# Performance work log

Measured on AMD Instinct MI355X. Metric: run time of the kernel, lower is better.

Reference implementation:

```python
import jax, jax.numpy as jnp
import numpy as np

IMAGE_SIZE = 256
NEAR = 0.1
FAR = 100.0
EPS = 1e-3
BACKGROUND = (0.0, 0.0, 0.0)
CHUNK = 64   # faces per scan step (bounds peak memory of the z-buffer pass)
TINY = 1e-12


def _bary(vx, vy, vz, xp, yp):
    """Barycentric weights / perspective-correct depth at pixel centers.
    vx, vy, vz: 3-tuples of vertex coords, broadcastable with xp/yp.
    Mirrors the CUDA kernel: unnormalized cross-product weights, normalize,
    clamp to [0,1], renormalize, zp = 1 / sum(w_k / z_k), near/far clip."""
    x0, x1, x2 = vx; y0, y1, y2 = vy; z0, z1, z2 = vz
    w0 = yp * (x2 - x1) + xp * (y1 - y2) + (x1 * y2 - x2 * y1)
    w1 = yp * (x0 - x2) + xp * (y2 - y0) + (x2 * y0 - x0 * y2)
    w2 = yp * (x1 - x0) + xp * (y0 - y1) + (x0 * y1 - x1 * y0)
    det = w0 + w1 + w2
    safe_det = jnp.where(jnp.abs(det) > TINY, det, 1.0)
    n0, n1, n2 = w0 / safe_det, w1 / safe_det, w2 / safe_det
    inside = (n0 > 0) & (n1 > 0) & (n2 > 0) & (jnp.abs(det) > TINY)
    n0 = jnp.clip(n0, 0.0, 1.0); n1 = jnp.clip(n1, 0.0, 1.0); n2 = jnp.clip(n2, 0.0, 1.0)
    s = n0 + n1 + n2
    s = jnp.where(s > TINY, s, 1.0)
    n0, n1, n2 = n0 / s, n1 / s, n2 / s
    inv_zp = n0 / z0 + n1 / z1 + n2 / z2
    inv_zp = jnp.where(jnp.abs(inv_zp) > TINY, inv_zp, 1.0)
    zp = 1.0 / inv_zp
    valid = inside & (zp > NEAR) & (zp < FAR)
    return (n0, n1, n2), zp, valid


def _pixel_coords():
    IS = IMAGE_SIZE
    return (2.0 * jnp.arange(IS, dtype=jnp.float32) + 1.0 - IS) / IS


def _forward(faces, textures):
    B, F = faces.shape[:2]
    IS = IMAGE_SIZE
    ii = _pixel_coords()

    # ---- pass 1: z-buffer (face-index argmin), chunked scan over faces ----
    # index selection is non-differentiable -> stop_gradient keeps vjp cheap
    fsg = jax.lax.stop_gradient(faces)
    n_chunks = F // CHUNK
    fchunks = jnp.transpose(fsg.reshape(B, n_chunks, CHUNK, 3, 3), (1, 0, 2, 3, 4))
    bases = jnp.arange(n_chunks, dtype=jnp.int32) * CHUNK
    xp4 = ii[None, None, None, :]
    yp4 = ii[None, None, :, None]

    def step(carry, inp):
        depth, fidx = carry
        fc, base = inp                               # fc: [B, CHUNK, 3, 3]
        vx = tuple(fc[:, :, k, 0][:, :, None, None] for k in range(3))
        vy = tuple(fc[:, :, k, 1][:, :, None, None] for k in range(3))
        vz = tuple(fc[:, :, k, 2][:, :, None, None] for k in range(3))
        _, zp, valid = _bary(vx, vy, vz, xp4, yp4)   # [B, CHUNK, IS, IS]
        zp = jnp.where(valid, zp, jnp.inf)
        local = jnp.argmin(zp, axis=1).astype(jnp.int32)
        zbest = jnp.min(zp, axis=1)
        better = zbest < depth
        depth = jnp.where(better, zbest, depth)
        fidx = jnp.where(better, base + local, fidx)
        return (depth, fidx), None

    init = (jnp.full((B, IS, IS), FAR, jnp.float32),
            jnp.full((B, IS, IS), -1, jnp.int32))
    (_, fidx), _ = jax.lax.scan(step, init, (fchunks, bases))

    # ---- pass 2: differentiable recompute for winning faces ----
    mask = fidx >= 0
    safe_idx = jnp.maximum(fidx, 0)
    fsel = jnp.take_along_axis(
        faces.reshape(B, F, 9), safe_idx.reshape(B, -1, 1), axis=1
    ).reshape(B, IS, IS, 3, 3)
    vx = tuple(fsel[..., k, 0] for k in range(3))
    vy = tuple(fsel[..., k, 1] for k in range(3))
    vz = tuple(fsel[..., k, 2] for k in range(3))
    w, zp, _ = _bary(vx, vy, vz, ii[None, None, :], ii[None, :, None])
    depth_map = jnp.where(mask, zp, FAR)

    # ---- texture sampling: 8-corner trilinear in the T^3 face texel cube ----
    T = textures.shape[2]
    tif = [jnp.clip(w[k] * (T - 1) * zp / vz[k], 0.0, T - 1 - EPS) for k in range(3)]
    lo = [jnp.floor(t) for t in tif]
    fr = [t - l for t, l in zip(tif, lo)]
    lo = [l.astype(jnp.int32) for l in lo]

    tex_flat = textures.reshape(B, F * T * T * T, 3)
    base_idx = safe_idx * (T * T * T)
    rgb = jnp.zeros((B, IS, IS, 3), faces.dtype)
    for d0 in (0, 1):
        for d1 in (0, 1):
            for d2 in (0, 1):
                wgt = ((fr[0] if d0 else 1.0 - fr[0]) *
                       (fr[1] if d1 else 1.0 - fr[1]) *
                       (fr[2] if d2 else 1.0 - fr[2]))
                idx = base_idx + (lo[0] + d0) * T * T + (lo[1] + d1) * T + (lo[2] + d2)
                smp = jnp.take_along_axis(tex_flat, idx.reshape(B, -1, 1), axis=1)
                rgb = rgb + wgt[..., None] * smp.reshape(B, IS, IS, 3)

    bg = jnp.asarray(BACKGROUND, faces.dtype)
    mf = mask.astype(faces.dtype)[..., None]
    rgb_map = rgb * mf + (1.0 - mf) * bg
    alpha_map = mask.astype(faces.dtype)
    # pack (rgb, alpha, depth) into a single [B, IS, IS, 5] tensor
    return jnp.concatenate([rgb_map, alpha_map[..., None], depth_map[..., None]], axis=-1)


def setup_inputs() -> dict:
    key = jax.random.key(0)
    B, F, T = 4, 4096, 4
    k1, k2, k3, k4, k5 = jax.random.split(key, 5)
    # small triangles scattered over the screen with depths in (near, far)
    ctr = jax.random.uniform(k1, (B, F, 1, 2), minval=-0.95, maxval=0.95)
    off = jax.random.uniform(k2, (B, F, 3, 2), minval=-0.08, maxval=0.08)
    xy = ctr + off
    zc = jax.random.uniform(k3, (B, F, 1, 1), minval=1.0, maxval=50.0)
    zo = jax.random.uniform(k4, (B, F, 3, 1), minval=-0.2, maxval=0.2)
    faces = jnp.concatenate([xy, zc + zo], axis=-1).astype(jnp.float32)
    textures = jax.random.uniform(k5, (B, F, T, T, T, 3), dtype=jnp.float32)
    return {"faces": faces, "textures": textures}


def reference(faces, textures):
    return _forward(faces, textures)
```

## Files before the change

### kernel.cpp

```cpp
#include <hip/hip_runtime.h>

#define IS 256
#define FCOUNT 4096
#define NEARP 0.1f
#define FARP 100.0f
#define TINYF 1e-12f
#define CAP 192
#define GCAP 128
#define DET_GLOBAL 1e-5f
#define ZEPS 2e-4f

__device__ __forceinline__ float frn(float r) { asm("" : "+v"(r)); return r; }
__device__ __forceinline__ float mulrn(float a, float b) { return frn(a * b); }
__device__ __forceinline__ float addrn(float a, float b) { return frn(a + b); }
__device__ __forceinline__ float subrn(float a, float b) { return frn(a - b); }
__device__ __forceinline__ float divrn(float a, float b) { return frn(a / b); }
__device__ __forceinline__ float fmarn(float a, float b, float c) {
    return frn(__builtin_fmaf(a, b, c));
}


__global__ __launch_bounds__(64) void bin_kernel(
    const float* __restrict__ faces,
    float4* __restrict__ cA, float4* __restrict__ cB, float4* __restrict__ cC,
    int* __restrict__ counts, int* __restrict__ lists,
    int* __restrict__ gcount, int* __restrict__ glist, int B, int F)
{
    const int lane = threadIdx.x;
    const int base = blockIdx.x * 64;
    const int gid  = base + lane;
    if (gid >= B * F) return;
    const int b = gid >> 12, f = gid & (FCOUNT - 1);

    __shared__ float4 stage4[144];
    float* stage = (float*)stage4;
    const float* src = faces + (size_t)base * 9;
    const float4* s4 = (const float4*)src;
    stage4[lane]      = s4[lane];
    stage4[64 + lane] = s4[64 + lane];
    stage[512 + lane] = src[512 + lane];
    __builtin_amdgcn_wave_barrier();

    const float* fp = stage + lane * 9;
    const float x0 = fp[0], y0 = fp[1], z0 = fp[2];
    const float x1 = fp[3], y1 = fp[4], z1 = fp[5];
    const float x2 = fp[6], y2 = fp[7], z2 = fp[8];

    const float A0 = subrn(x2, x1), B0 = subrn(y1, y2);
    const float C0 = fmarn(x1, y2, -mulrn(x2, y1));
    const float A1 = subrn(x0, x2), B1 = subrn(y2, y0);
    const float C1 = fmarn(x2, y0, -mulrn(x0, y2));
    const float A2 = subrn(x1, x0), B2 = subrn(y0, y1);
    const float C2 = fmarn(x0, y1, -mulrn(x1, y0));
    cA[gid] = make_float4(A0, B0, C0, A1);
    cB[gid] = make_float4(B1, C1, A2, B2);
    cC[gid] = make_float4(C2, z0, z1, z2);

    const float det = (x1 - x0) * (y2 - y0) - (x2 - x0) * (y1 - y0);
    const float ad = fabsf(det);
    if (ad < DET_GLOBAL) {
        const int pos = atomicAdd(&gcount[b], 1);
        if (pos < GCAP) glist[b * GCAP + pos] = f;
        return;
    }
    const float d = 2e-3f + 3e-7f / ad;
    const float lox = fminf(x0, fminf(x1, x2)) - d;
    const float hix = fmaxf(x0, fmaxf(x1, x2)) + d;
    const float loy = fminf(y0, fminf(y1, y2)) - d;
    const float hiy = fmaxf(y0, fmaxf(y1, y2)) + d;
    int tx0 = (int)ceilf ((256.f * lox + 241.f) * (1.f / 16.f));
    int tx1 = (int)floorf((256.f * hix + 255.f) * (1.f / 16.f));
    int ty0 = (int)ceilf ((256.f * loy + 241.f) * (1.f / 16.f));
    int ty1 = (int)floorf((256.f * hiy + 255.f) * (1.f / 16.f));
    tx0 = max(tx0, 0); tx1 = min(tx1, 31);
    ty0 = max(ty0, 0); ty1 = min(ty1, 31);
    for (int ty = ty0; ty <= ty1; ++ty)
        for (int tx = tx0; tx <= tx1; ++tx) {
            const int t = (b * 32 + ty) * 32 + tx;
            const int pos = atomicAdd(&counts[t], 1);
            if (pos < CAP) lists[(size_t)t * CAP + pos] = f;
        }
}

__global__ __launch_bounds__(64) void raster_kernel(
    const float* __restrict__ textures,
    const float4* __restrict__ cA, const float4* __restrict__ cB,
    const float4* __restrict__ cC,
    const int* __restrict__ counts, const int* __restrict__ lists,
    const int* __restrict__ gcount, const int* __restrict__ glist,
    float* __restrict__ out, int B, int F)
{
    const int lane = threadIdx.x;
    const int blk  = blockIdx.x;
    const int b    = blk >> 10;
    const int tx   = blk & 31;
    const int ty   = (blk >> 5) & 31;
    const int bin  = (b * 32 + ty) * 32 + tx;
    const int px   = tx * 8 + (lane & 7);
    const int py   = ty * 8 + (lane >> 3);
    const float xp = (float)(2 * px + 1 - IS) * (1.0f / IS);
    const float yp = (float)(2 * py + 1 - IS) * (1.0f / IS);

    const int cnt   = min(counts[bin], CAP);
    const int gcnt  = min(gcount[b], GCAP);
    const int total = cnt + gcnt;
    const int* mylist = lists + (size_t)bin * CAP;
    const int* gl     = glist + b * GCAP;
    const int fb = b * F;

    float bestz = FARP;
    int   besti = -1;
    float bn0 = 0.f, bn1 = 0.f, bn2 = 0.f;
    float bz0 = 1.f, bz1 = 1.f, bz2 = 1.f;

    int    pf = 0;
    float4 pa, pb, pc;
    if (total > 0) {
        pf = (0 < cnt) ? mylist[0] : gl[0];
        pa = cA[fb + pf]; pb = cB[fb + pf]; pc = cC[fb + pf];
    }
    for (int j = 0; j < total; ++j) {
        const float4 fa  = pa;
        const float4 fb4 = pb;
        const float4 fc  = pc;
        const int    fi  = pf;
        const int jn = j + 1;
        if (jn < total) {
            pf = (jn < cnt) ? mylist[jn] : gl[jn - cnt];
            pa = cA[fb + pf]; pb = cB[fb + pf]; pc = cC[fb + pf];
        }
        const float w0 = addrn(fmarn(yp, fa.x, mulrn(xp, fa.y)), fa.z);
        const float w1 = addrn(fmarn(yp, fa.w, mulrn(xp, fb4.x)), fb4.y);
        const float w2 = addrn(fmarn(yp, fb4.z, mulrn(xp, fb4.w)), fc.x);
        const float det = addrn(addrn(w0, w1), w2);
        bool ins;
        if (det > TINYF)       ins = (w0 > 0.f) && (w1 > 0.f) && (w2 > 0.f);
        else if (det < -TINYF) ins = (w0 < 0.f) && (w1 < 0.f) && (w2 < 0.f);
        else                   ins = false;
        const float minz = fminf(fminf(fc.y, fc.z), fc.w);
        if (ins && minz <= bestz + ZEPS) {
            float n0 = divrn(w0, det), n1 = divrn(w1, det), n2 = divrn(w2, det);
            n0 = frn(fminf(fmaxf(n0, 0.f), 1.f));
            n1 = frn(fminf(fmaxf(n1, 0.f), 1.f));
            n2 = frn(fminf(fmaxf(n2, 0.f), 1.f));
            float s = addrn(addrn(n0, n1), n2);
            s = (s > TINYF) ? s : 1.0f;
            n0 = divrn(n0, s); n1 = divrn(n1, s); n2 = divrn(n2, s);
            float iz = addrn(addrn(divrn(n0, fc.y), divrn(n1, fc.z)),
                             divrn(n2, fc.w));
            iz = (fabsf(iz) > TINYF) ? iz : 1.0f;
            const float zp = divrn(1.0f, iz);
            if (zp > NEARP && zp < FARP) {
                if (zp < bestz || (zp == bestz && fi < besti)) {
                    bestz = zp;
                    besti = fi;
                    bn0 = n0; bn1 = n1; bn2 = n2;
                    bz0 = fc.y; bz1 = fc.z; bz2 = fc.w;
                }
            }
        }
    }

    float r = 0.f, g = 0.f, bch = 0.f, alpha = 0.f, depth = FARP;
    if (besti >= 0) {
        const float zp = bestz;
        depth = zp;
        const float t0 = fminf(fmaxf(divrn(mulrn(mulrn(bn0, 3.0f), zp), bz0), 0.f), 2.999f);
        const float t1 = fminf(fmaxf(divrn(mulrn(mulrn(bn1, 3.0f), zp), bz1), 0.f), 2.999f);
        const float t2 = fminf(fmaxf(divrn(mulrn(mulrn(bn2, 3.0f), zp), bz2), 0.f), 2.999f);
        const float l0 = floorf(t0), l1 = floorf(t1), l2 = floorf(t2);
        const float fr0 = subrn(t0, l0), fr1 = subrn(t1, l1), fr2 = subrn(t2, l2);
        const int i0 = (int)l0, i1 = (int)l1, i2 = (int)l2;

        const float* txp = textures + (size_t)(b * F + besti) * 64 * 3;
        for (int d0 = 0; d0 < 2; ++d0)
            for (int d1 = 0; d1 < 2; ++d1)
                for (int d2 = 0; d2 < 2; ++d2) {
                    const float wg = mulrn(mulrn(d0 ? fr0 : subrn(1.0f, fr0),
                                                 d1 ? fr1 : subrn(1.0f, fr1)),
                                           d2 ? fr2 : subrn(1.0f, fr2));
                    const float* tp = txp + ((i0 + d0) * 16 + (i1 + d1) * 4 + (i2 + d2)) * 3;
                    r   = addrn(r,   mulrn(wg, tp[0]));
                    g   = addrn(g,   mulrn(wg, tp[1]));
                    bch = addrn(bch, mulrn(wg, tp[2]));
                }
        alpha = 1.0f;
    }

    float* op = out + (((size_t)b * IS + py) * IS + px) * 5;
    op[0] = r;
    op[1] = g;
    op[2] = bch;
    op[3] = alpha;
    op[4] = depth;
}

extern "C" void kernel_launch(void* const* d_in, const int* in_sizes, int n_in,
                              void* d_out, int out_size, void* d_ws, size_t ws_size,
                              hipStream_t stream) {
    const float* faces    = (const float*)d_in[0];
    const float* textures = (const float*)d_in[1];
    float* out = (float*)d_out;
    const int F = FCOUNT;
    const int B = in_sizes[0] / (F * 9);
    const int nbins = B * 1024;

    int* counts = (int*)d_ws;
    int* gcount = counts + nbins;
    int* glist  = gcount + B;
    int* lists  = glist + B * GCAP;
    float4* cA  = (float4*)(lists + (size_t)nbins * CAP);
    float4* cB  = cA + (size_t)B * F;
    float4* cC  = cB + (size_t)B * F;

    hipMemsetAsync(counts, 0, (size_t)(nbins + B) * sizeof(int), stream);
    bin_kernel<<<dim3((B * F + 63) / 64), dim3(64), 0, stream>>>(
        faces, cA, cB, cC, counts, lists, gcount, glist, B, F);
    raster_kernel<<<dim3(B * 1024), dim3(64), 0, stream>>>(
        textures, cA, cB, cC, counts, lists, gcount, glist, out, B, F);
}
```

Before: 103.7 us.

## Split per-tile face list across four waves and merge depth winners in shared memory

The raster kernel now runs four wavefronts per 8x8 tile. Each wave scans every fourth face in the bin list and keeps its own best depth. The per-wave winners go to LDS, and wave 0 reduces them with the same tie-break on lower face index, then does texture sampling and output. This shortens the serial per-pixel loop over candidate faces. The cost is a block barrier, LDS traffic, and idle waves during shading. The early-out on bestz is also weaker, since each wave only sees its own subset of faces.

```diff
diff --git a/kernel.cpp b/kernel.cpp
--- a/kernel.cpp
+++ b/kernel.cpp
@@ -82,7 +82,7 @@
         }
 }
 
-__global__ __launch_bounds__(64) void raster_kernel(
+__global__ __launch_bounds__(256, 8) void raster_kernel(
     const float* __restrict__ textures,
     const float4* __restrict__ cA, const float4* __restrict__ cB,
     const float4* __restrict__ cC,
@@ -90,7 +90,9 @@
     const int* __restrict__ gcount, const int* __restrict__ glist,
     float* __restrict__ out, int B, int F)
 {
-    const int lane = threadIdx.x;
+    const int tid  = threadIdx.x;
+    const int lane = tid & 63;
+    const int w    = tid >> 6;
     const int blk  = blockIdx.x;
     const int b    = blk >> 10;
     const int tx   = blk & 31;
@@ -101,6 +103,11 @@
     const float xp = (float)(2 * px + 1 - IS) * (1.0f / IS);
     const float yp = (float)(2 * py + 1 - IS) * (1.0f / IS);
 
+    __shared__ float s_pz[4][64];
+    __shared__ int   s_pi[4][64];
+    __shared__ float s_pn[4][64][3];
+    __shared__ float s_pvz[4][64][3];
+
     const int cnt   = min(counts[bin], CAP);
     const int gcnt  = min(gcount[b], GCAP);
     const int total = cnt + gcnt;
@@ -115,16 +122,16 @@
 
     int    pf = 0;
     float4 pa, pb, pc;
-    if (total > 0) {
-        pf = (0 < cnt) ? mylist[0] : gl[0];
+    if (w < total) {
+        pf = (w < cnt) ? mylist[w] : gl[w - cnt];
         pa = cA[fb + pf]; pb = cB[fb + pf]; pc = cC[fb + pf];
     }
-    for (int j = 0; j < total; ++j) {
+    for (int j = w; j < total; j += 4) {
         const float4 fa  = pa;
         const float4 fb4 = pb;
         const float4 fc  = pc;
         const int    fi  = pf;
-        const int jn = j + 1;
+        const int jn = j + 4;
         if (jn < total) {
             pf = (jn < cnt) ? mylist[jn] : gl[jn - cnt];
             pa = cA[fb + pf]; pb = cB[fb + pf]; pc = cC[fb + pf];
@@ -161,38 +168,62 @@
         }
     }
 
-    float r = 0.f, g = 0.f, bch = 0.f, alpha = 0.f, depth = FARP;
-    if (besti >= 0) {
-        const float zp = bestz;
-        depth = zp;
-        const float t0 = fminf(fmaxf(divrn(mulrn(mulrn(bn0, 3.0f), zp), bz0), 0.f), 2.999f);
-        const float t1 = fminf(fmaxf(divrn(mulrn(mulrn(bn1, 3.0f), zp), bz1), 0.f), 2.999f);
-        const float t2 = fminf(fmaxf(divrn(mulrn(mulrn(bn2, 3.0f), zp), bz2), 0.f), 2.999f);
-        const float l0 = floorf(t0), l1 = floorf(t1), l2 = floorf(t2);
-        const float fr0 = subrn(t0, l0), fr1 = subrn(t1, l1), fr2 = subrn(t2, l2);
-        const int i0 = (int)l0, i1 = (int)l1, i2 = (int)l2;
-
-        const float* txp = textures + (size_t)(b * F + besti) * 64 * 3;
-        for (int d0 = 0; d0 < 2; ++d0)
-            for (int d1 = 0; d1 < 2; ++d1)
-                for (int d2 = 0; d2 < 2; ++d2) {
-                    const float wg = mulrn(mulrn(d0 ? fr0 : subrn(1.0f, fr0),
-                                                 d1 ? fr1 : subrn(1.0f, fr1)),
-                                           d2 ? fr2 : subrn(1.0f, fr2));
-                    const float* tp = txp + ((i0 + d0) * 16 + (i1 + d1) * 4 + (i2 + d2)) * 3;
-                    r   = addrn(r,   mulrn(wg, tp[0]));
-                    g   = addrn(g,   mulrn(wg, tp[1]));
-                    bch = addrn(bch, mulrn(wg, tp[2]));
-                }
-        alpha = 1.0f;
-    }
-
-    float* op = out + (((size_t)b * IS + py) * IS + px) * 5;
-    op[0] = r;
-    op[1] = g;
-    op[2] = bch;
-    op[3] = alpha;
-    op[4] = depth;
+    s_pz[w][lane] = bestz;
+    s_pi[w][lane] = besti;
+    s_pn[w][lane][0]  = bn0; s_pn[w][lane][1]  = bn1; s_pn[w][lane][2]  = bn2;
+    s_pvz[w][lane][0] = bz0; s_pvz[w][lane][1] = bz1; s_pvz[w][lane][2] = bz2;
+    __syncthreads();
+
+    if (w == 0) {
+        float z = s_pz[0][lane];
+        int   i = s_pi[0][lane];
+        int  ws = 0;
+        #pragma unroll
+        for (int s = 1; s < 4; ++s) {
+            const float zs = s_pz[s][lane];
+            const int   is = s_pi[s][lane];
+            if (zs < z || (zs == z && is < i)) { z = zs; i = is; ws = s; }
+        }
+
+        float r = 0.f, g = 0.f, bch = 0.f, alpha = 0.f, depth = FARP;
+        if (i >= 0) {
+            const float n0 = s_pn[ws][lane][0];
+            const float n1 = s_pn[ws][lane][1];
+            const float n2 = s_pn[ws][lane][2];
+            const float z0 = s_pvz[ws][lane][0];
+            const float z1 = s_pvz[ws][lane][1];
+            const float z2 = s_pvz[ws][lane][2];
+            const float zp = z;
+            depth = zp;
+            const float t0 = fminf(fmaxf(divrn(mulrn(mulrn(n0, 3.0f), zp), z0), 0.f), 2.999f);
+            const float t1 = fminf(fmaxf(divrn(mulrn(mulrn(n1, 3.0f), zp), z1), 0.f), 2.999f);
+            const float t2 = fminf(fmaxf(divrn(mulrn(mulrn(n2, 3.0f), zp), z2), 0.f), 2.999f);
+            const float l0 = floorf(t0), l1 = floorf(t1), l2 = floorf(t2);
+            const float fr0 = subrn(t0, l0), fr1 = subrn(t1, l1), fr2 = subrn(t2, l2);
+            const int i0 = (int)l0, i1 = (int)l1, i2 = (int)l2;
+
+            const float* txp = textures + (size_t)(b * F + i) * 64 * 3;
+            for (int d0 = 0; d0 < 2; ++d0)
+                for (int d1 = 0; d1 < 2; ++d1)
+                    for (int d2 = 0; d2 < 2; ++d2) {
+                        const float wg = mulrn(mulrn(d0 ? fr0 : subrn(1.0f, fr0),
+                                                     d1 ? fr1 : subrn(1.0f, fr1)),
+                                               d2 ? fr2 : subrn(1.0f, fr2));
+                        const float* tp = txp + ((i0 + d0) * 16 + (i1 + d1) * 4 + (i2 + d2)) * 3;
+                        r   = addrn(r,   mulrn(wg, tp[0]));
+                        g   = addrn(g,   mulrn(wg, tp[1]));
+                        bch = addrn(bch, mulrn(wg, tp[2]));
+                    }
+            alpha = 1.0f;
+        }
+
+        float* op = out + (((size_t)b * IS + py) * IS + px) * 5;
+        op[0] = r;
+        op[1] = g;
+        op[2] = bch;
+        op[3] = alpha;
+        op[4] = depth;
+    }
 }
 
 extern "C" void kernel_launch(void* const* d_in, const int* in_sizes, int n_in,
@@ -216,6 +247,6 @@
     hipMemsetAsync(counts, 0, (size_t)(nbins + B) * sizeof(int), stream);
     bin_kernel<<<dim3((B * F + 63) / 64), dim3(64), 0, stream>>>(
         faces, cA, cB, cC, counts, lists, gcount, glist, B, F);
-    raster_kernel<<<dim3(B * 1024), dim3(64), 0, stream>>>(
+    raster_kernel<<<dim3(B * 1024), dim3(256), 0, stream>>>(
         textures, cA, cB, cC, counts, lists, gcount, glist, out, B, F);
 }
```

Result: faster. 101.5 us (-2.1%).
